# Optimization experiments

Measured on AMD Instinct MI355X. Metric: run time of the kernel, lower is better.

The kernel has to match this reference:

```python
import jax, jax.numpy as jnp
import numpy as np

B, N, PL = 8, 961, 50          # batch, sequence_len=(64-4)//2+1 squared, patch_len=3*4^2+2
HID = 200                       # int(4.0 * patch_len)
D, H, HD = 768, 12, 64          # embed_dim, num_heads, head_dim
MP = 1536                       # int(2.0 * embed_dim)


def setup_inputs() -> dict:
    key = jax.random.key(0)
    ks = jax.random.split(key, 16)
    w = lambda k, i, o: jax.random.normal(k, (i, o), jnp.float32) / np.float32(np.sqrt(i))
    b = lambda k, o: jax.random.normal(k, (o,), jnp.float32) * np.float32(0.01)
    return {
        "x": jax.random.normal(ks[0], (B, N, PL), jnp.float32),
        "W1": w(ks[1], PL, HID),   "b1": b(ks[2], HID),
        "W2": w(ks[3], HID, HID),  "b2": b(ks[4], HID),
        "W3": w(ks[5], HID, HID),  "b3": b(ks[6], HID),
        "W4": w(ks[7], HID, D),    "b4": b(ks[8], D),
        "Wruv": w(ks[9], D, 3 * D), "bruv": b(ks[10], 3 * D),
        "Wp1": w(ks[11], N * HD, MP), "bp1": b(ks[12], MP),
        "Wp2": w(ks[13], MP, 1),      "bp2": b(ks[14], 1),
    }


def reference(x, W1, b1, W2, b2, W3, b3, W4, b4, Wruv, bruv, Wp1, bp1, Wp2, bp2):
    Bs, Ns, _ = x.shape
    # pointwise MLP (note: original has NO activations, just stacked Linears)
    h = x.reshape(Bs * Ns, -1)
    h = (((h @ W1 + b1) @ W2 + b2) @ W3 + b3) @ W4 + b4           # (B*N, D)
    # fused r,u,v projection -> (3, H, B, N, HD)
    ruv = (h @ Wruv + bruv).reshape(Bs, Ns, 3, H, HD).transpose(2, 3, 0, 1, 4)
    r, u, v = ruv[0], ruv[1], ruv[2]                               # each (H, B, N, HD)
    attn = jax.nn.softmax(jnp.einsum('hbnd,hbmd->hbnm', r, u), axis=-1)
    o = jnp.einsum('hbnm,hbmd->hbnd', attn, v).reshape(H, Bs, Ns * HD)
    # per-head projection: weights are SHARED across heads (list built via [m]*H)
    q = (jnp.einsum('hbm,mp->hbp', o, Wp1) + bp1) @ Wp2 + bp2      # (H, B, 1)
    return q[..., 0].T                                             # (B, 12)
```

## Files before the change

kernel.cpp:

```cpp
#include <hip/hip_runtime.h>
#include <hip/hip_bf16.h>

#define TPB 256

typedef __attribute__((ext_vector_type(8))) short bf16x8;
typedef __attribute__((ext_vector_type(4))) float f32x4;

static __device__ __forceinline__ unsigned short f2bf(float f) {
  union { float f; unsigned int u; } x; x.f = f;
  unsigned int r = x.u + 0x7FFF + ((x.u >> 16) & 1);
  return (unsigned short)(r >> 16);
}
static __device__ __forceinline__ float bf2f(unsigned short h) {
  union { unsigned int u; float f; } x; x.u = ((unsigned int)h) << 16;
  return x.f;
}

#define MFMA16(a, b, c) __builtin_amdgcn_mfma_f32_16x16x32_bf16(a, b, c, 0, 0, 0)

__global__ __launch_bounds__(TPB) void fold_wp_fused_k(
    const float* __restrict__ A, const float* __restrict__ lastrow,
    const float* __restrict__ W, const float* __restrict__ bias,
    float* __restrict__ C, int K, int Nc, int gemmBlocks,
    const float* __restrict__ Wp1, const float* __restrict__ Wp2,
    float* __restrict__ wfold, int wpStart, int wpCount,
    const float* __restrict__ bp1, const float* __restrict__ bp2,
    float* __restrict__ out)
{
  __shared__ float As[64][68];
  __shared__ float Ws[64][68];
  __shared__ float red[4];
  int bid = blockIdx.x, tid = threadIdx.x;

  if (bid >= gemmBlocks) {
    int u = bid - gemmBlocks;
    int wv = tid >> 6, lane = tid & 63;
    if (u >= wpCount) {
      float s = 0.f;
      for (int i = tid; i < 1536; i += TPB) s += bp1[i] * Wp2[i];
#pragma unroll
      for (int off = 32; off >= 1; off >>= 1) s += __shfl_xor(s, off, 64);
      if (lane == 0) red[wv] = s;
      __syncthreads();
      if (tid < 96) out[tid] = red[0] + red[1] + red[2] + red[3] + bp2[0];
      return;
    }
    float* w2 = &As[0][0];
    for (int i = tid; i < 1536; i += TPB) w2[i] = Wp2[i];
    __syncthreads();
    int m = (wpStart + u) * 4 + wv;
    const float* row = Wp1 + (size_t)m * 1536;
    float s = 0.f;
#pragma unroll
    for (int k = 0; k < 6; ++k) {
      float4 a  = *(const float4*)(row + k * 256 + lane * 4);
      float4 ww = *(const float4*)&w2[k * 256 + lane * 4];
      s += a.x * ww.x + a.y * ww.y + a.z * ww.z + a.w * ww.w;
    }
#pragma unroll
    for (int off = 32; off >= 1; off >>= 1) s += __shfl_xor(s, off, 64);
    if (lane == 0) wfold[m] = s;
    return;
  }

  int col0 = bid * 64;
  int ty = tid >> 4, tx = tid & 15;
  float acc[4][4] = {};
  for (int k0 = 0; k0 < K; k0 += 64) {
#pragma unroll
    for (int i = 0; i < 16; ++i) {
      int idx = tid + i * TPB;
      int r = idx >> 6, kk = idx & 63;
      int gk = k0 + kk;
      float v = 0.f;
      if (gk < K) {
        if (r < 50) v = A[(size_t)r * K + gk];
        else if (r == 50) v = lastrow[gk];
      }
      As[kk][r] = v;
    }
#pragma unroll
    for (int i = 0; i < 16; ++i) {
      int idx = tid + i * TPB;
      int kk = idx >> 6, cc = idx & 63;
      int gk = k0 + kk, gc = col0 + cc;
      float v = 0.f;
      if (gk < K && gc < Nc) v = W[(size_t)gk * Nc + gc];
      Ws[kk][cc] = v;
    }
    __syncthreads();
#pragma unroll 8
    for (int kk = 0; kk < 64; ++kk) {
      float4 a4 = *(const float4*)&As[kk][ty * 4];
      float4 b4 = *(const float4*)&Ws[kk][tx * 4];
      float av[4] = {a4.x, a4.y, a4.z, a4.w};
      float bv[4] = {b4.x, b4.y, b4.z, b4.w};
#pragma unroll
      for (int i = 0; i < 4; ++i)
#pragma unroll
        for (int j = 0; j < 4; ++j)
          acc[i][j] = fmaf(av[i], bv[j], acc[i][j]);
    }
    __syncthreads();
  }
#pragma unroll
  for (int i = 0; i < 4; ++i) {
    int gr = ty * 4 + i;
    if (gr >= 51) continue;
#pragma unroll
    for (int j = 0; j < 4; ++j) {
      int gc = col0 + tx * 4 + j;
      if (gc >= Nc) continue;
      float v = acc[i][j];
      if (gr == 50) v += bias[gc];
      C[(size_t)gr * Nc + gc] = v;
    }
  }
}

__global__ __launch_bounds__(TPB) void fold4_fused_k(
    const float* __restrict__ aug3,
    const float* __restrict__ Wruv,
    const float* __restrict__ bruv,
    unsigned short* __restrict__ WfTh, unsigned short* __restrict__ WfTl,
    float* __restrict__ bfv,
    const float* __restrict__ x,
    unsigned short* __restrict__ xh, unsigned short* __restrict__ xl,
    const float* __restrict__ Wp1, const float* __restrict__ Wp2,
    float* __restrict__ wfold, int wpStart, int wpCount)
{
  __shared__ float As[64][68];
  __shared__ float Ws[64][68];
  int bid = blockIdx.x, tid = threadIdx.x;

  if (bid >= 157) {
    int u = bid - 157;
    if (u >= wpCount) return;
    int wv = tid >> 6, lane = tid & 63;
    float* w2 = &As[0][0];
    for (int i = tid; i < 1536; i += TPB) w2[i] = Wp2[i];
    __syncthreads();
    int m = (wpStart + u) * 4 + wv;
    const float* row = Wp1 + (size_t)m * 1536;
    float s = 0.f;
#pragma unroll
    for (int k = 0; k < 6; ++k) {
      float4 a  = *(const float4*)(row + k * 256 + lane * 4);
      float4 ww = *(const float4*)&w2[k * 256 + lane * 4];
      s += a.x * ww.x + a.y * ww.y + a.z * ww.z + a.w * ww.w;
    }
#pragma unroll
    for (int off = 32; off >= 1; off >>= 1) s += __shfl_xor(s, off, 64);
    if (lane == 0) wfold[m] = s;
    return;
  }

  if (bid >= 36) {
    int row0 = (bid - 36) * 64;
#pragma unroll
    for (int i = 0; i < 16; ++i) {
      int idx = tid + i * TPB;
      int row = row0 + (idx >> 6), cc = idx & 63;
      if (row >= 7688) continue;
      float v = (cc < 50) ? x[(size_t)row * 50 + cc] : 0.f;
      unsigned short hi = f2bf(v);
      xh[(size_t)row * 64 + cc] = hi;
      xl[(size_t)row * 64 + cc] = f2bf(v - bf2f(hi));
    }
    return;
  }

  const int K = 768, Nc = 2304;
  const float* lastrow = aug3 + (size_t)50 * 768;
  int col0 = bid * 64;
  int ty = tid >> 4, tx = tid & 15;
  float acc[4][4] = {};
  for (int k0 = 0; k0 < K; k0 += 64) {
#pragma unroll
    for (int i = 0; i < 16; ++i) {
      int idx = tid + i * TPB;
      int r = idx >> 6, kk = idx & 63;
      int gk = k0 + kk;
      float v = 0.f;
      if (r < 50) v = aug3[(size_t)r * K + gk];
      else if (r == 50) v = lastrow[gk];
      As[kk][r] = v;
    }
#pragma unroll
    for (int i = 0; i < 16; ++i) {
      int idx = tid + i * TPB;
      int kk = idx >> 6, cc = idx & 63;
      Ws[kk][cc] = Wruv[(size_t)(k0 + kk) * Nc + col0 + cc];
    }
    __syncthreads();
#pragma unroll 8
    for (int kk = 0; kk < 64; ++kk) {
      float4 a4 = *(const float4*)&As[kk][ty * 4];
      float4 b4 = *(const float4*)&Ws[kk][tx * 4];
      float av[4] = {a4.x, a4.y, a4.z, a4.w};
      float bv[4] = {b4.x, b4.y, b4.z, b4.w};
#pragma unroll
      for (int i = 0; i < 4; ++i)
#pragma unroll
        for (int j = 0; j < 4; ++j)
          acc[i][j] = fmaf(av[i], bv[j], acc[i][j]);
    }
    __syncthreads();
  }
#pragma unroll
  for (int i = 0; i < 4; ++i) {
    int gr = ty * 4 + i;
    if (gr >= 51) continue;
#pragma unroll
    for (int j = 0; j < 4; ++j) {
      int gc = col0 + tx * 4 + j;
      float v = acc[i][j];
      if (gr == 50) {
        bfv[gc] = v + bruv[gc];
      } else {
        unsigned short hi = f2bf(v);
        size_t el = (size_t)gc * 64 + gr;
        WfTh[el] = hi;
        WfTl[el] = f2bf(v - bf2f(hi));
      }
    }
  }
}

__global__ __launch_bounds__(TPB) void gemm_ruv_mfma_k(
    const unsigned short* __restrict__ xh,
    const unsigned short* __restrict__ xl,
    const unsigned short* __restrict__ WfTh,
    const unsigned short* __restrict__ WfTl,
    const float* __restrict__ bias,
    unsigned short* __restrict__ RU,
    unsigned short* __restrict__ Vt)
{
  int tid = threadIdx.x, w = tid >> 6, lane = tid & 63;
  int g = lane >> 4, c = lane & 15;
  int by = blockIdx.y;
  int b = by >> 4, nb = by & 15;
  int m0 = b * 961 + nb * 64;
  int n0base = nb * 64;
  int col0 = blockIdx.x * 256;
  int wc0 = w * 64;

  bf16x8 afh[4][2], afl[4][2];
#pragma unroll
  for (int rt = 0; rt < 4; ++rt) {
    size_t rowb = (size_t)(m0 + rt * 16 + c) * 64;
#pragma unroll
    for (int kk = 0; kk < 2; ++kk) {
      afh[rt][kk] = *(const bf16x8*)&xh[rowb + kk * 32 + g * 8];
      afl[rt][kk] = *(const bf16x8*)&xl[rowb + kk * 32 + g * 8];
    }
  }

  f32x4 zero4 = {0.f, 0.f, 0.f, 0.f};
  f32x4 acc[4][4] = {{zero4, zero4, zero4, zero4}, {zero4, zero4, zero4, zero4},
                     {zero4, zero4, zero4, zero4}, {zero4, zero4, zero4, zero4}};

#pragma unroll
  for (int ct = 0; ct < 4; ++ct) {
    size_t bcolb = (size_t)(col0 + wc0 + ct * 16 + c) * 64;
    bf16x8 bh0 = *(const bf16x8*)&WfTh[bcolb + g * 8];
    bf16x8 bh1 = *(const bf16x8*)&WfTh[bcolb + 32 + g * 8];
    bf16x8 bl0 = *(const bf16x8*)&WfTl[bcolb + g * 8];
    bf16x8 bl1 = *(const bf16x8*)&WfTl[bcolb + 32 + g * 8];
#pragma unroll
    for (int rt = 0; rt < 4; ++rt) {
      acc[rt][ct] = MFMA16(afh[rt][0], bh0, acc[rt][ct]);
      acc[rt][ct] = MFMA16(afh[rt][1], bh1, acc[rt][ct]);
      acc[rt][ct] = MFMA16(afl[rt][0], bh0, acc[rt][ct]);
      acc[rt][ct] = MFMA16(afl[rt][1], bh1, acc[rt][ct]);
      acc[rt][ct] = MFMA16(afh[rt][0], bl0, acc[rt][ct]);
      acc[rt][ct] = MFMA16(afh[rt][1], bl1, acc[rt][ct]);
    }
  }

  bool isRU = (col0 < 1536);
#pragma unroll
  for (int ct = 0; ct < 4; ++ct) {
    int col = col0 + wc0 + ct * 16 + c;
    float bs = bias[col];
    if (isRU) {
#pragma unroll
      for (int rt = 0; rt < 4; ++rt) {
        int lr0 = rt * 16 + g * 4;
#pragma unroll
        for (int r = 0; r < 4; ++r) {
          int n = n0base + lr0 + r;
          if (n <= 960)
            RU[(size_t)(m0 + lr0 + r) * 1536 + col] = f2bf(acc[rt][ct][r] + bs);
        }
      }
    } else {
      int hd = col - 1536;
      int hh = hd >> 6, d = hd & 63;
      size_t vrow = ((size_t)(hh * 8 + b) * 64 + d) * 968;
#pragma unroll
      for (int rt = 0; rt < 4; ++rt) {
        int n0 = n0base + rt * 16 + g * 4;
        if (n0 + 3 <= 960) {
          ushort4 o;
          o.x = f2bf(acc[rt][ct][0] + bs);
          o.y = f2bf(acc[rt][ct][1] + bs);
          o.z = f2bf(acc[rt][ct][2] + bs);
          o.w = f2bf(acc[rt][ct][3] + bs);
          *(ushort4*)&Vt[vrow + n0] = o;
        } else {
#pragma unroll
          for (int r = 0; r < 4; ++r) {
            int n = n0 + r;
            if (n <= 960) Vt[vrow + n] = f2bf(acc[rt][ct][r] + bs);
          }
        }
      }
    }
  }
}

__global__ __launch_bounds__(512) void attn_final_k(
    const unsigned short* __restrict__ RU,
    const unsigned short* __restrict__ Vt,
    const float* __restrict__ wfold,
    float* __restrict__ out)
{
  __shared__ unsigned short sh[24576];
  int bid = blockIdx.x;
  int tid = threadIdx.x;

  const int NS = 961, RS = 1536, VROW = 968;
  int qb = bid & 7, hb = bid >> 3;
  int h = hb >> 3, b = hb & 7;
  int n0 = qb * 128;
  int w = tid >> 6, lane = tid & 63;
  int g = lane >> 4, c = lane & 15;
  const unsigned short* rubase = RU + (size_t)b * NS * RS;
  int roff = h * 64, uoff = 768 + h * 64;
  const unsigned short* vtbase = Vt + (size_t)hb * 64 * VROW;
  unsigned short* Kbuf[2] = {sh, sh + 4096};
  unsigned short* Vbuf[2] = {sh + 8192, sh + 12288};
  unsigned short* pw = sh + 16384 + w * 1024;

  int qrow = n0 + w * 16 + c;
  if (qrow > 960) qrow = 960;
  bf16x8 qf0 = *(const bf16x8*)(rubase + (size_t)qrow * RS + roff + g * 8);
  bf16x8 qf1 = *(const bf16x8*)(rubase + (size_t)qrow * RS + roff + 32 + g * 8);

  bf16x8 ones;
#pragma unroll
  for (int i = 0; i < 8; ++i) ones[i] = (short)0x3F80;

  int srow = tid >> 3, ss = tid & 7;
  int sel = srow * 64 + 8 * (ss ^ (srow & 7));
  const unsigned short* ksrc = rubase + uoff + ss * 8;
  const unsigned short* vsrc = vtbase + (size_t)srow * VROW + ss * 8;

  {
    int4 kv = *(const int4*)(ksrc + (size_t)srow * RS);
    int4 vv = *(const int4*)(vsrc);
    *(int4*)&Kbuf[0][sel] = kv;
    *(int4*)&Vbuf[0][sel] = vv;
  }
  __syncthreads();

  f32x4 zero4 = {0.f, 0.f, 0.f, 0.f};
  f32x4 oacc[4] = {zero4, zero4, zero4, zero4};
  f32x4 rowacc = zero4;

  unsigned short* Kc = Kbuf[0];
  unsigned short* Vc = Vbuf[0];
  unsigned short* Kn = Kbuf[1];
  unsigned short* Vn = Vbuf[1];

  for (int kt = 0; kt < 16; ++kt) {
    int4 pk, pv;
    bool pre = (kt < 15);
    if (pre) {
      int keyg = (kt + 1) * 64 + srow;
      int kcl = keyg > 960 ? 960 : keyg;
      pk = *(const int4*)(ksrc + (size_t)kcl * RS);
      pv = *(const int4*)(vsrc + (kt + 1) * 64);
    }

    f32x4 sa[4] = {zero4, zero4, zero4, zero4};
    __builtin_amdgcn_s_setprio(1);
#pragma unroll
    for (int ct = 0; ct < 4; ++ct) {
      int key = c * 4 + ct;
      int sw = (key & 7) * 8;
      bf16x8 k0 = *(const bf16x8*)&Kc[key * 64 + ((g * 8) ^ sw)];
      bf16x8 k1 = *(const bf16x8*)&Kc[key * 64 + ((32 + g * 8) ^ sw)];
      sa[ct] = MFMA16(qf0, k0, sa[ct]);
      sa[ct] = MFMA16(qf1, k1, sa[ct]);
    }
    __builtin_amdgcn_s_setprio(0);

    if (kt < 15) {
#pragma unroll
      for (int r = 0; r < 4; ++r) {
        unsigned short pb[4];
#pragma unroll
        for (int ct = 0; ct < 4; ++ct)
          pb[ct] = f2bf(__expf(sa[ct][r]));
        int q = g * 4 + r;
        int e0 = (c * 4) ^ ((q & 7) * 8);
        *(unsigned int*)&pw[q * 64 + e0] =
            (unsigned int)pb[0] | ((unsigned int)pb[1] << 16);
        *(unsigned int*)&pw[q * 64 + e0 + 2] =
            (unsigned int)pb[2] | ((unsigned int)pb[3] << 16);
      }
    } else {
#pragma unroll
      for (int r = 0; r < 4; ++r) {
        unsigned short pb[4];
#pragma unroll
        for (int ct = 0; ct < 4; ++ct) {
          int keyg = kt * 64 + c * 4 + ct;
          pb[ct] = (keyg <= 960) ? f2bf(__expf(sa[ct][r])) : (unsigned short)0;
        }
        int q = g * 4 + r;
        int e0 = (c * 4) ^ ((q & 7) * 8);
        *(unsigned int*)&pw[q * 64 + e0] =
            (unsigned int)pb[0] | ((unsigned int)pb[1] << 16);
        *(unsigned int*)&pw[q * 64 + e0 + 2] =
            (unsigned int)pb[2] | ((unsigned int)pb[3] << 16);
      }
    }

    if (pre) {
      *(int4*)&Kn[sel] = pk;
      *(int4*)&Vn[sel] = pv;
    }

    __builtin_amdgcn_s_setprio(1);
#pragma unroll
    for (int kk = 0; kk < 2; ++kk) {
      bf16x8 pa = *(const bf16x8*)&pw[c * 64 + ((kk * 32 + g * 8) ^ ((c & 7) * 8))];
      rowacc = MFMA16(pa, ones, rowacc);
#pragma unroll
      for (int dt = 0; dt < 4; ++dt) {
        int d = dt * 16 + c;
        bf16x8 vf = *(const bf16x8*)&Vc[d * 64 + ((kk * 32 + g * 8) ^ ((d & 7) * 8))];
        oacc[dt] = MFMA16(pa, vf, oacc[dt]);
      }
    }
    __builtin_amdgcn_s_setprio(0);

    __syncthreads();
    unsigned short* t;
    t = Kc; Kc = Kn; Kn = t;
    t = Vc; Vc = Vn; Vn = t;
  }

  int nbase = n0 + w * 16 + g * 4;
  float part = 0.f;
#pragma unroll
  for (int r = 0; r < 4; ++r) {
    int n = nbase + r;
    if (n > 960) continue;
    float inv = 1.f / rowacc[r];
#pragma unroll
    for (int dt = 0; dt < 4; ++dt)
      part += oacc[dt][r] * inv * wfold[(size_t)n * 64 + dt * 16 + c];
  }
#pragma unroll
  for (int off = 32; off >= 1; off >>= 1) part += __shfl_xor(part, off, 64);
  float* red = (float*)sh;
  if (lane == 0) red[w] = part;
  __syncthreads();
  if (tid == 0) {
    float tot = red[0] + red[1] + red[2] + red[3] +
                red[4] + red[5] + red[6] + red[7];
    atomicAdd(&out[b * 12 + h], tot);
  }
}

extern "C" void kernel_launch(void* const* d_in, const int* in_sizes, int n_in,
                              void* d_out, int out_size, void* d_ws, size_t ws_size,
                              hipStream_t stream)
{
  const float* x    = (const float*)d_in[0];
  const float* W1   = (const float*)d_in[1];
  const float* b1   = (const float*)d_in[2];
  const float* W2   = (const float*)d_in[3];
  const float* b2   = (const float*)d_in[4];
  const float* W3   = (const float*)d_in[5];
  const float* b3   = (const float*)d_in[6];
  const float* W4   = (const float*)d_in[7];
  const float* b4   = (const float*)d_in[8];
  const float* Wruv = (const float*)d_in[9];
  const float* bruv = (const float*)d_in[10];
  const float* Wp1  = (const float*)d_in[11];
  const float* bp1  = (const float*)d_in[12];
  const float* Wp2  = (const float*)d_in[13];
  const float* bp2  = (const float*)d_in[14];
  float* out = (float*)d_out;

  char* base = (char*)d_ws;
  size_t off = 0;
  auto alloc = [&](size_t bytes) -> void* {
    void* p = base + off;
    off = (off + bytes + 255) & ~(size_t)255;
    return p;
  };
  unsigned short* RU  = (unsigned short*)alloc((size_t)7688 * 1536 * 2);
  unsigned short* Vt  = (unsigned short*)alloc((size_t)96 * 64 * 968 * 2 + 1024);
  float* aug1  = (float*)alloc(51 * 200 * 4);
  float* aug2  = (float*)alloc(51 * 200 * 4);
  float* aug3  = (float*)alloc(51 * 768 * 4);
  unsigned short* WfTh = (unsigned short*)alloc((size_t)2304 * 64 * 2);
  unsigned short* WfTl = (unsigned short*)alloc((size_t)2304 * 64 * 2);
  unsigned short* xh   = (unsigned short*)alloc((size_t)(7688 + 64) * 64 * 2);
  unsigned short* xl   = (unsigned short*)alloc((size_t)(7688 + 64) * 64 * 2);
  float* bfv   = (float*)alloc(2304 * 4);
  float* wfold = (float*)alloc(61504 * 4);
  if (off > ws_size) return;

  dim3 tb(TPB);

  fold_wp_fused_k<<<dim3(4 + 3000 + 1), tb, 0, stream>>>(
      W1, b1, W2, b2, aug1, 200, 200, 4,
      Wp1, Wp2, wfold, 0, 3000, bp1, bp2, out);
  fold_wp_fused_k<<<dim3(4 + 3000), tb, 0, stream>>>(
      aug1, aug1 + 50 * 200, W3, b3, aug2, 200, 200, 4,
      Wp1, Wp2, wfold, 3000, 3000, bp1, bp2, out);
  fold_wp_fused_k<<<dim3(12 + 3000), tb, 0, stream>>>(
      aug2, aug2 + 50 * 200, W4, b4, aug3, 200, 768, 12,
      Wp1, Wp2, wfold, 6000, 3000, bp1, bp2, out);

  fold4_fused_k<<<dim3(157 + 6376), tb, 0, stream>>>(
      aug3, Wruv, bruv, WfTh, WfTl, bfv, x, xh, xl,
      Wp1, Wp2, wfold, 9000, 6376);

  gemm_ruv_mfma_k<<<dim3(9, 128), tb, 0, stream>>>(xh, xl, WfTh, WfTl, bfv, RU, Vt);

  attn_final_k<<<dim3(768), dim3(512), 0, stream>>>(RU, Vt, wfold, out);
}
```

Baseline: 329.8 us.

## Fold R/U/V projections into per-head bilinear form on augmented input x

Drops the full RUV GEMM. Scores are computed as x·(Wr Wu^T)·x^T, using a per-head 64x64 matrix M built from the folded weights, with the bias carried by a constant-1 augmented column. The value projection is folded into the output weights (wvf), so attention runs directly over the 64-wide augmented x and its transpose xT. This removes the large RU/Vt intermediate writes and reads, at the cost of a small prep kernel. It also rounds x to bf16 for the K/V operands and the Z=xM product to bf16, which may change precision.

```diff
diff --git a/kernel.cpp b/kernel.cpp
--- a/kernel.cpp
+++ b/kernel.cpp
@@ -126,6 +126,7 @@
     float* __restrict__ bfv,
     const float* __restrict__ x,
     unsigned short* __restrict__ xh, unsigned short* __restrict__ xl,
+    unsigned short* __restrict__ xT,
     const float* __restrict__ Wp1, const float* __restrict__ Wp2,
     float* __restrict__ wfold, int wpStart, int wpCount)
 {
@@ -162,10 +163,15 @@
       int idx = tid + i * TPB;
       int row = row0 + (idx >> 6), cc = idx & 63;
       if (row >= 7688) continue;
-      float v = (cc < 50) ? x[(size_t)row * 50 + cc] : 0.f;
+      float v = 0.f;
+      if (cc < 50) v = x[(size_t)row * 50 + cc];
+      else if (cc == 50) v = 1.0f;
       unsigned short hi = f2bf(v);
       xh[(size_t)row * 64 + cc] = hi;
       xl[(size_t)row * 64 + cc] = f2bf(v - bf2f(hi));
+      int bb = row / 961;
+      int nl = row - bb * 961;
+      xT[((size_t)bb * 64 + cc) * 968 + nl] = hi;
     }
     return;
   }
@@ -227,146 +233,155 @@
   }
 }
 
-__global__ __launch_bounds__(TPB) void gemm_ruv_mfma_k(
+__global__ __launch_bounds__(TPB) void prep_k(
+    const unsigned short* __restrict__ WfTh,
+    const unsigned short* __restrict__ WfTl,
+    const float* __restrict__ bfv,
+    const float* __restrict__ wfold,
+    unsigned short* __restrict__ Mth,
+    unsigned short* __restrict__ Mtl,
+    float* __restrict__ wvf)
+{
+  __shared__ float Al[64][64];
+  __shared__ float Bl[64][64];
+  int bid = blockIdx.x, tid = threadIdx.x;
+
+  if (bid < 12) {
+    int h = bid;
+    for (int idx = tid; idx < 4096; idx += TPB) {
+      int d = idx >> 6, i = idx & 63;
+      int colr = h * 64 + d, colu = 768 + h * 64 + d;
+      float wr = 0.f, wu = 0.f;
+      if (i < 50) {
+        wr = bf2f(WfTh[(size_t)colr * 64 + i]) + bf2f(WfTl[(size_t)colr * 64 + i]);
+        wu = bf2f(WfTh[(size_t)colu * 64 + i]) + bf2f(WfTl[(size_t)colu * 64 + i]);
+      } else if (i == 50) {
+        wr = bfv[colr];
+        wu = bfv[colu];
+      }
+      Al[d][i] = wr;
+      Bl[d][i] = wu;
+    }
+    __syncthreads();
+    for (int idx = tid; idx < 4096; idx += TPB) {
+      int j = idx >> 6, i = idx & 63;
+      float m = 0.f;
+#pragma unroll 8
+      for (int d = 0; d < 64; ++d) m += Al[d][i] * Bl[d][j];
+      unsigned short hi = f2bf(m);
+      size_t el = ((size_t)h * 64 + j) * 64 + i;
+      Mth[el] = hi;
+      Mtl[el] = f2bf(m - bf2f(hi));
+    }
+    return;
+  }
+
+  int u = bid - 12;
+  int h = u >> 4, nb = u & 15;
+  for (int idx = tid; idx < 4096; idx += TPB) {
+    int d = idx >> 6, f = idx & 63;
+    int colv = 1536 + h * 64 + d;
+    float wv = 0.f;
+    if (f < 50)
+      wv = bf2f(WfTh[(size_t)colv * 64 + f]) + bf2f(WfTl[(size_t)colv * 64 + f]);
+    else if (f == 50)
+      wv = bfv[colv];
+    Al[d][f] = wv;
+    int nl = idx >> 6, dd = idx & 63;
+    int n = nb * 64 + nl;
+    Bl[nl][dd] = (n <= 960) ? wfold[(size_t)n * 64 + dd] : 0.f;
+  }
+  __syncthreads();
+  for (int idx = tid; idx < 4096; idx += TPB) {
+    int nl = idx >> 6, f = idx & 63;
+    int n = nb * 64 + nl;
+    if (n > 960) continue;
+    float s = 0.f;
+#pragma unroll 8
+    for (int d = 0; d < 64; ++d) s += Bl[nl][d] * Al[d][f];
+    wvf[((size_t)h * 961 + n) * 64 + f] = s;
+  }
+}
+
+__global__ __launch_bounds__(512) void attn_x_k(
     const unsigned short* __restrict__ xh,
     const unsigned short* __restrict__ xl,
-    const unsigned short* __restrict__ WfTh,
-    const unsigned short* __restrict__ WfTl,
-    const float* __restrict__ bias,
-    unsigned short* __restrict__ RU,
-    unsigned short* __restrict__ Vt)
-{
-  int tid = threadIdx.x, w = tid >> 6, lane = tid & 63;
-  int g = lane >> 4, c = lane & 15;
-  int by = blockIdx.y;
-  int b = by >> 4, nb = by & 15;
-  int m0 = b * 961 + nb * 64;
-  int n0base = nb * 64;
-  int col0 = blockIdx.x * 256;
-  int wc0 = w * 64;
-
-  bf16x8 afh[4][2], afl[4][2];
-#pragma unroll
-  for (int rt = 0; rt < 4; ++rt) {
-    size_t rowb = (size_t)(m0 + rt * 16 + c) * 64;
-#pragma unroll
-    for (int kk = 0; kk < 2; ++kk) {
-      afh[rt][kk] = *(const bf16x8*)&xh[rowb + kk * 32 + g * 8];
-      afl[rt][kk] = *(const bf16x8*)&xl[rowb + kk * 32 + g * 8];
-    }
-  }
-
-  f32x4 zero4 = {0.f, 0.f, 0.f, 0.f};
-  f32x4 acc[4][4] = {{zero4, zero4, zero4, zero4}, {zero4, zero4, zero4, zero4},
-                     {zero4, zero4, zero4, zero4}, {zero4, zero4, zero4, zero4}};
-
-#pragma unroll
-  for (int ct = 0; ct < 4; ++ct) {
-    size_t bcolb = (size_t)(col0 + wc0 + ct * 16 + c) * 64;
-    bf16x8 bh0 = *(const bf16x8*)&WfTh[bcolb + g * 8];
-    bf16x8 bh1 = *(const bf16x8*)&WfTh[bcolb + 32 + g * 8];
-    bf16x8 bl0 = *(const bf16x8*)&WfTl[bcolb + g * 8];
-    bf16x8 bl1 = *(const bf16x8*)&WfTl[bcolb + 32 + g * 8];
-#pragma unroll
-    for (int rt = 0; rt < 4; ++rt) {
-      acc[rt][ct] = MFMA16(afh[rt][0], bh0, acc[rt][ct]);
-      acc[rt][ct] = MFMA16(afh[rt][1], bh1, acc[rt][ct]);
-      acc[rt][ct] = MFMA16(afl[rt][0], bh0, acc[rt][ct]);
-      acc[rt][ct] = MFMA16(afl[rt][1], bh1, acc[rt][ct]);
-      acc[rt][ct] = MFMA16(afh[rt][0], bl0, acc[rt][ct]);
-      acc[rt][ct] = MFMA16(afh[rt][1], bl1, acc[rt][ct]);
-    }
-  }
-
-  bool isRU = (col0 < 1536);
-#pragma unroll
-  for (int ct = 0; ct < 4; ++ct) {
-    int col = col0 + wc0 + ct * 16 + c;
-    float bs = bias[col];
-    if (isRU) {
-#pragma unroll
-      for (int rt = 0; rt < 4; ++rt) {
-        int lr0 = rt * 16 + g * 4;
-#pragma unroll
-        for (int r = 0; r < 4; ++r) {
-          int n = n0base + lr0 + r;
-          if (n <= 960)
-            RU[(size_t)(m0 + lr0 + r) * 1536 + col] = f2bf(acc[rt][ct][r] + bs);
-        }
-      }
-    } else {
-      int hd = col - 1536;
-      int hh = hd >> 6, d = hd & 63;
-      size_t vrow = ((size_t)(hh * 8 + b) * 64 + d) * 968;
-#pragma unroll
-      for (int rt = 0; rt < 4; ++rt) {
-        int n0 = n0base + rt * 16 + g * 4;
-        if (n0 + 3 <= 960) {
-          ushort4 o;
-          o.x = f2bf(acc[rt][ct][0] + bs);
-          o.y = f2bf(acc[rt][ct][1] + bs);
-          o.z = f2bf(acc[rt][ct][2] + bs);
-          o.w = f2bf(acc[rt][ct][3] + bs);
-          *(ushort4*)&Vt[vrow + n0] = o;
-        } else {
-#pragma unroll
-          for (int r = 0; r < 4; ++r) {
-            int n = n0 + r;
-            if (n <= 960) Vt[vrow + n] = f2bf(acc[rt][ct][r] + bs);
-          }
-        }
-      }
-    }
-  }
-}
-
-__global__ __launch_bounds__(512) void attn_final_k(
-    const unsigned short* __restrict__ RU,
-    const unsigned short* __restrict__ Vt,
-    const float* __restrict__ wfold,
+    const unsigned short* __restrict__ xT,
+    const unsigned short* __restrict__ Mth,
+    const unsigned short* __restrict__ Mtl,
+    const float* __restrict__ wvf,
     float* __restrict__ out)
 {
   __shared__ unsigned short sh[24576];
   int bid = blockIdx.x;
   int tid = threadIdx.x;
 
-  const int NS = 961, RS = 1536, VROW = 968;
   int qb = bid & 7, hb = bid >> 3;
   int h = hb >> 3, b = hb & 7;
   int n0 = qb * 128;
   int w = tid >> 6, lane = tid & 63;
   int g = lane >> 4, c = lane & 15;
-  const unsigned short* rubase = RU + (size_t)b * NS * RS;
-  int roff = h * 64, uoff = 768 + h * 64;
-  const unsigned short* vtbase = Vt + (size_t)hb * 64 * VROW;
+  int xb = b * 961;
   unsigned short* Kbuf[2] = {sh, sh + 4096};
   unsigned short* Vbuf[2] = {sh + 8192, sh + 12288};
   unsigned short* pw = sh + 16384 + w * 1024;
 
+  int srow = tid >> 3, ss = tid & 7;
+  int sel = srow * 64 + 8 * (ss ^ (srow & 7));
+  const unsigned short* ksrc = xh + (size_t)xb * 64 + ss * 8;
+  const unsigned short* vsrc = xT + ((size_t)b * 64 + srow) * 968 + ss * 8;
+  int4 kv0 = *(const int4*)(ksrc + (size_t)srow * 64);
+  int4 vv0 = *(const int4*)(vsrc);
+
   int qrow = n0 + w * 16 + c;
   if (qrow > 960) qrow = 960;
-  bf16x8 qf0 = *(const bf16x8*)(rubase + (size_t)qrow * RS + roff + g * 8);
-  bf16x8 qf1 = *(const bf16x8*)(rubase + (size_t)qrow * RS + roff + 32 + g * 8);
+  size_t rowb = (size_t)(xb + qrow) * 64;
+  bf16x8 axh0 = *(const bf16x8*)&xh[rowb + g * 8];
+  bf16x8 axh1 = *(const bf16x8*)&xh[rowb + 32 + g * 8];
+  bf16x8 axl0 = *(const bf16x8*)&xl[rowb + g * 8];
+  bf16x8 axl1 = *(const bf16x8*)&xl[rowb + 32 + g * 8];
+
+  f32x4 zero4 = {0.f, 0.f, 0.f, 0.f};
+  f32x4 zacc[4] = {zero4, zero4, zero4, zero4};
+#pragma unroll
+  for (int ct = 0; ct < 4; ++ct) {
+    int j = c * 4 + ct;
+    size_t mb = ((size_t)h * 64 + j) * 64;
+    bf16x8 bh0 = *(const bf16x8*)&Mth[mb + g * 8];
+    bf16x8 bh1 = *(const bf16x8*)&Mth[mb + 32 + g * 8];
+    bf16x8 bl0 = *(const bf16x8*)&Mtl[mb + g * 8];
+    bf16x8 bl1 = *(const bf16x8*)&Mtl[mb + 32 + g * 8];
+    zacc[ct] = MFMA16(axh0, bh0, zacc[ct]);
+    zacc[ct] = MFMA16(axh1, bh1, zacc[ct]);
+    zacc[ct] = MFMA16(axl0, bh0, zacc[ct]);
+    zacc[ct] = MFMA16(axl1, bh1, zacc[ct]);
+    zacc[ct] = MFMA16(axh0, bl0, zacc[ct]);
+    zacc[ct] = MFMA16(axh1, bl1, zacc[ct]);
+  }
+#pragma unroll
+  for (int r = 0; r < 4; ++r) {
+    unsigned short pb[4];
+#pragma unroll
+    for (int ct = 0; ct < 4; ++ct) pb[ct] = f2bf(zacc[ct][r]);
+    int q = g * 4 + r;
+    int e0 = (c * 4) ^ ((q & 7) * 8);
+    *(unsigned int*)&pw[q * 64 + e0] =
+        (unsigned int)pb[0] | ((unsigned int)pb[1] << 16);
+    *(unsigned int*)&pw[q * 64 + e0 + 2] =
+        (unsigned int)pb[2] | ((unsigned int)pb[3] << 16);
+  }
+  bf16x8 zf0 = *(const bf16x8*)&pw[c * 64 + ((g * 8) ^ ((c & 7) * 8))];
+  bf16x8 zf1 = *(const bf16x8*)&pw[c * 64 + ((32 + g * 8) ^ ((c & 7) * 8))];
 
   bf16x8 ones;
 #pragma unroll
   for (int i = 0; i < 8; ++i) ones[i] = (short)0x3F80;
 
-  int srow = tid >> 3, ss = tid & 7;
-  int sel = srow * 64 + 8 * (ss ^ (srow & 7));
-  const unsigned short* ksrc = rubase + uoff + ss * 8;
-  const unsigned short* vsrc = vtbase + (size_t)srow * VROW + ss * 8;
-
-  {
-    int4 kv = *(const int4*)(ksrc + (size_t)srow * RS);
-    int4 vv = *(const int4*)(vsrc);
-    *(int4*)&Kbuf[0][sel] = kv;
-    *(int4*)&Vbuf[0][sel] = vv;
-  }
+  *(int4*)&Kbuf[0][sel] = kv0;
+  *(int4*)&Vbuf[0][sel] = vv0;
   __syncthreads();
 
-  f32x4 zero4 = {0.f, 0.f, 0.f, 0.f};
-  f32x4 oacc[4] = {zero4, zero4, zero4, zero4};
+  f32x4 pxacc[4] = {zero4, zero4, zero4, zero4};
   f32x4 rowacc = zero4;
 
   unsigned short* Kc = Kbuf[0];
@@ -380,7 +395,7 @@
     if (pre) {
       int keyg = (kt + 1) * 64 + srow;
       int kcl = keyg > 960 ? 960 : keyg;
-      pk = *(const int4*)(ksrc + (size_t)kcl * RS);
+      pk = *(const int4*)(ksrc + (size_t)kcl * 64);
       pv = *(const int4*)(vsrc + (kt + 1) * 64);
     }
 
@@ -392,8 +407,8 @@
       int sw = (key & 7) * 8;
       bf16x8 k0 = *(const bf16x8*)&Kc[key * 64 + ((g * 8) ^ sw)];
       bf16x8 k1 = *(const bf16x8*)&Kc[key * 64 + ((32 + g * 8) ^ sw)];
-      sa[ct] = MFMA16(qf0, k0, sa[ct]);
-      sa[ct] = MFMA16(qf1, k1, sa[ct]);
+      sa[ct] = MFMA16(zf0, k0, sa[ct]);
+      sa[ct] = MFMA16(zf1, k1, sa[ct]);
     }
     __builtin_amdgcn_s_setprio(0);
 
@@ -443,7 +458,7 @@
       for (int dt = 0; dt < 4; ++dt) {
         int d = dt * 16 + c;
         bf16x8 vf = *(const bf16x8*)&Vc[d * 64 + ((kk * 32 + g * 8) ^ ((d & 7) * 8))];
-        oacc[dt] = MFMA16(pa, vf, oacc[dt]);
+        pxacc[dt] = MFMA16(pa, vf, pxacc[dt]);
       }
     }
     __builtin_amdgcn_s_setprio(0);
@@ -461,9 +476,10 @@
     int n = nbase + r;
     if (n > 960) continue;
     float inv = 1.f / rowacc[r];
+    const float* wv = wvf + ((size_t)h * 961 + n) * 64;
 #pragma unroll
     for (int dt = 0; dt < 4; ++dt)
-      part += oacc[dt][r] * inv * wfold[(size_t)n * 64 + dt * 16 + c];
+      part += pxacc[dt][r] * inv * wv[dt * 16 + c];
   }
 #pragma unroll
   for (int off = 32; off >= 1; off >>= 1) part += __shfl_xor(part, off, 64);
@@ -505,8 +521,6 @@
     off = (off + bytes + 255) & ~(size_t)255;
     return p;
   };
-  unsigned short* RU  = (unsigned short*)alloc((size_t)7688 * 1536 * 2);
-  unsigned short* Vt  = (unsigned short*)alloc((size_t)96 * 64 * 968 * 2 + 1024);
   float* aug1  = (float*)alloc(51 * 200 * 4);
   float* aug2  = (float*)alloc(51 * 200 * 4);
   float* aug3  = (float*)alloc(51 * 768 * 4);
@@ -514,6 +528,10 @@
   unsigned short* WfTl = (unsigned short*)alloc((size_t)2304 * 64 * 2);
   unsigned short* xh   = (unsigned short*)alloc((size_t)(7688 + 64) * 64 * 2);
   unsigned short* xl   = (unsigned short*)alloc((size_t)(7688 + 64) * 64 * 2);
+  unsigned short* xT   = (unsigned short*)alloc((size_t)8 * 64 * 968 * 2 + 1024);
+  unsigned short* Mth  = (unsigned short*)alloc((size_t)12 * 64 * 64 * 2);
+  unsigned short* Mtl  = (unsigned short*)alloc((size_t)12 * 64 * 64 * 2);
+  float* wvf   = (float*)alloc((size_t)12 * 961 * 64 * 4);
   float* bfv   = (float*)alloc(2304 * 4);
   float* wfold = (float*)alloc(61504 * 4);
   if (off > ws_size) return;
@@ -531,10 +549,10 @@
       Wp1, Wp2, wfold, 6000, 3000, bp1, bp2, out);
 
   fold4_fused_k<<<dim3(157 + 6376), tb, 0, stream>>>(
-      aug3, Wruv, bruv, WfTh, WfTl, bfv, x, xh, xl,
+      aug3, Wruv, bruv, WfTh, WfTl, bfv, x, xh, xl, xT,
       Wp1, Wp2, wfold, 9000, 6376);
 
-  gemm_ruv_mfma_k<<<dim3(9, 128), tb, 0, stream>>>(xh, xl, WfTh, WfTl, bfv, RU, Vt);
-
-  attn_final_k<<<dim3(768), dim3(512), 0, stream>>>(RU, Vt, wfold, out);
-}
+  prep_k<<<dim3(204), tb, 0, stream>>>(WfTh, WfTl, bfv, wfold, Mth, Mtl, wvf);
+
+  attn_x_k<<<dim3(768), dim3(512), 0, stream>>>(xh, xl, xT, Mth, Mtl, wvf, out);
+}
```

New measurement: 318.6 us. 1.04x faster.
